# Optimization experiments

Hardware: AMD Instinct MI355X
Metric: run time of the kernel (lower is better)

## Reference

```python
import jax, jax.numpy as jnp
import numpy as np

HEADS = 16
LN_EPS = 1e-5

def _ln(v, w, b):
    # LayerNorm over last dim (head dim s)
    mu = jnp.mean(v, axis=-1, keepdims=True)
    var = jnp.mean(jnp.square(v - mu), axis=-1, keepdims=True)
    return (v - mu) * jax.lax.rsqrt(var + LN_EPS) * w + b

def setup_inputs() -> dict:
    key = jax.random.key(0)
    ks = jax.random.split(key, 5)
    b, t, e = 2, 2048, 1024
    x = jax.random.normal(ks[0], (b, t, e), dtype=jnp.float32)
    scale = 0.02
    Wk = jax.random.normal(ks[1], (e, e), dtype=jnp.float32) * scale
    Wq = jax.random.normal(ks[2], (e, e), dtype=jnp.float32) * scale
    Wv = jax.random.normal(ks[3], (e, e), dtype=jnp.float32) * scale
    Wu = jax.random.normal(ks[4], (e, e), dtype=jnp.float32) * scale
    s = e // HEADS
    return {
        "x": x, "Wk": Wk, "Wq": Wq, "Wv": Wv, "Wu": Wu,
        "kln_w": jnp.ones((s,), jnp.float32), "kln_b": jnp.zeros((s,), jnp.float32),
        "qln_w": jnp.ones((s,), jnp.float32), "qln_b": jnp.zeros((s,), jnp.float32),
    }

def reference(x, Wk, Wq, Wv, Wu, kln_w, kln_b, qln_w, qln_b):
    b, t, e = x.shape
    h = HEADS
    s = e // h
    # nn.Linear: y = x @ W^T
    k = (x @ Wk.T).reshape(b, t, h, s)
    q = (x @ Wq.T).reshape(b, t, h, s)
    v = (x @ Wv.T).reshape(b, t, h, s)
    k = _ln(k, kln_w, kln_b)
    q = _ln(q, qln_w, qln_b)
    scalefactor = 1.0 / np.sqrt(s).astype(np.float32)
    # [b, h, t_q, t_k]
    dot = jnp.einsum('bqhs,bkhs->bhqk', q, k) * scalefactor
    causal = jnp.triu(jnp.ones((t, t), dtype=bool), k=1)  # mask strictly-upper (diag kept)
    dot = jnp.where(causal, -jnp.inf, dot)
    attn = jax.nn.softmax(dot, axis=-1)
    out = jnp.einsum('bhqk,bkhs->bqhs', attn, v).reshape(b, t, e)
    return out @ Wu.T
```

## Files before the change

kernel.cpp:

```cpp
#include <hip/hip_runtime.h>
#include <math.h>

#define T_SEQ 2048
#define E_DIM 1024
#define NH    16
#define HS    64
#define NB    2
#define M_ROWS 4096

typedef __attribute__((ext_vector_type(8))) short bf16x8;
typedef __attribute__((ext_vector_type(4))) float f32x4;

#define AS1 __attribute__((address_space(1)))
#define AS3 __attribute__((address_space(3)))

#define LOG2E 1.4426950408889634f

__device__ __forceinline__ ushort f2bf(float f) {
    union { float f; unsigned u; } c; c.f = f;
    unsigned r = c.u + 0x7fffu + ((c.u >> 16) & 1u);
    return (ushort)(r >> 16);
}
__device__ __forceinline__ ushort f2bf_trunc(float f) {
    union { float f; unsigned u; } c; c.f = f;
    return (ushort)(c.u >> 16);
}

__device__ __forceinline__ void load_lds16(const ushort* g, ushort* l) {
    __builtin_amdgcn_global_load_lds((const AS1 unsigned int*)g,
                                     (AS3 unsigned int*)l, 16, 0, 0);
}

__global__ __launch_bounds__(256) void cvt_all(
    const float* __restrict__ x,  const float* __restrict__ Wk,
    const float* __restrict__ Wq, const float* __restrict__ Wv,
    const float* __restrict__ Wu,
    ushort* __restrict__ xb,  ushort* __restrict__ Wkb,
    ushort* __restrict__ Wqb, ushort* __restrict__ Wvb,
    ushort* __restrict__ Wub)
{
    int i4 = blockIdx.x * 256 + threadIdx.x;
    int region = i4 >> 18;
    const float* src; ushort* dst; int off;
    if      (region < 4)  { src = x;  dst = xb;  off = i4; }
    else if (region == 4) { src = Wk; dst = Wkb; off = i4 - (4 << 18); }
    else if (region == 5) { src = Wq; dst = Wqb; off = i4 - (5 << 18); }
    else if (region == 6) { src = Wv; dst = Wvb; off = i4 - (6 << 18); }
    else                  { src = Wu; dst = Wub; off = i4 - (7 << 18); }
    float4 v = *(const float4*)(src + (size_t)off * 4);
    ushort4 o; o.x = f2bf(v.x); o.y = f2bf(v.y); o.z = f2bf(v.z); o.w = f2bf(v.w);
    *(ushort4*)(dst + (size_t)off * 4) = o;
}

__device__ __forceinline__ void gemm_core64(
    const ushort* __restrict__ A, const ushort* __restrict__ W,
    int m0, int n0, ushort* As, ushort* Bs, f32x4 acc[2][4])
{
    const int tid  = threadIdx.x;
    const int lane = tid & 63, w = tid >> 6;
    const int quad = lane >> 4, l16 = lane & 15;

    const int rl   = lane >> 2;
    const int gsw  = (lane & 3) ^ ((lane >> 3) & 3);
    const int fsw  = (l16 >> 1) & 3;

    const f32x4 zero = {0.f, 0.f, 0.f, 0.f};
#pragma unroll
    for (int mt = 0; mt < 2; ++mt)
#pragma unroll
        for (int nt = 0; nt < 4; ++nt) acc[mt][nt] = zero;

    for (int k0 = 0; k0 < E_DIM; k0 += 32) {
#pragma unroll
        for (int i = 0; i < 2; ++i) {
            int c = w + i * 4;
            int row = c * 16 + rl;
            load_lds16(A + (size_t)(m0 + row) * E_DIM + k0 + gsw * 8, As + c * 512);
        }
        {
            int row = w * 16 + rl;
            load_lds16(W + (size_t)(n0 + row) * E_DIM + k0 + gsw * 8, Bs + w * 512);
        }
        __syncthreads();
        bf16x8 af[2], bfr[4];
#pragma unroll
        for (int mt = 0; mt < 2; ++mt)
            af[mt] = *(const bf16x8*)(As + (w * 32 + mt * 16 + l16) * 32
                                      + ((quad ^ fsw) * 8));
#pragma unroll
        for (int nt = 0; nt < 4; ++nt)
            bfr[nt] = *(const bf16x8*)(Bs + (nt * 16 + l16) * 32
                                       + ((quad ^ fsw) * 8));
#pragma unroll
        for (int mt = 0; mt < 2; ++mt)
#pragma unroll
            for (int nt = 0; nt < 4; ++nt)
                acc[mt][nt] = __builtin_amdgcn_mfma_f32_16x16x32_bf16(
                    af[mt], bfr[nt], acc[mt][nt], 0, 0, 0);
        __syncthreads();
    }
}

__global__ __launch_bounds__(256) void gemm_qkv(
    const ushort* __restrict__ A,
    const ushort* __restrict__ W0, const ushort* __restrict__ W1,
    const ushort* __restrict__ W2,
    ushort* __restrict__ Kb, ushort* __restrict__ Qb, ushort* __restrict__ Vt,
    const float* __restrict__ kw, const float* __restrict__ kbias,
    const float* __restrict__ qw, const float* __restrict__ qbias)
{
    __shared__ ushort As[128 * 32];
    __shared__ ushort Bs[64 * 32];
    const int n0g = blockIdx.x * 64;
    const int z   = n0g >> 10;
    const int n0  = n0g & 1023;
    const int m0  = blockIdx.y * 128;
    const ushort* W = (z == 0) ? W0 : (z == 1) ? W1 : W2;

    f32x4 acc[2][4];
    gemm_core64(A, W, m0, n0, As, Bs, acc);

    const int lane = threadIdx.x & 63, w = threadIdx.x >> 6;
    const int quad = lane >> 4, l16 = lane & 15;
    const int row0 = m0 + w * 32;

    if (z < 2) {
        ushort* C = z ? Qb : Kb;
        const float* lw = z ? qw : kw;
        const float* lb = z ? qbias : kbias;
        const float scale = z ? (0.125f * LOG2E) : 1.0f;
        float wv[4], bv_[4];
#pragma unroll
        for (int nt = 0; nt < 4; ++nt) {
            wv[nt]  = lw[nt * 16 + l16];
            bv_[nt] = lb[nt * 16 + l16];
        }
#pragma unroll
        for (int mt = 0; mt < 2; ++mt)
#pragma unroll
            for (int r = 0; r < 4; ++r) {
                float v[4], d[4];
#pragma unroll
                for (int nt = 0; nt < 4; ++nt) v[nt] = acc[mt][nt][r];
                float s = v[0] + v[1] + v[2] + v[3];
                s += __shfl_xor(s, 1); s += __shfl_xor(s, 2);
                s += __shfl_xor(s, 4); s += __shfl_xor(s, 8);
                float mu = s * (1.0f / 64.0f);
                float q2 = 0.f;
#pragma unroll
                for (int nt = 0; nt < 4; ++nt) { d[nt] = v[nt] - mu; q2 += d[nt] * d[nt]; }
                q2 += __shfl_xor(q2, 1); q2 += __shfl_xor(q2, 2);
                q2 += __shfl_xor(q2, 4); q2 += __shfl_xor(q2, 8);
                float rin = rsqrtf(q2 * (1.0f / 64.0f) + 1e-5f);
                int row = row0 + mt * 16 + quad * 4 + r;
#pragma unroll
                for (int nt = 0; nt < 4; ++nt)
                    C[(size_t)row * E_DIM + n0 + nt * 16 + l16] =
                        f2bf((d[nt] * rin * wv[nt] + bv_[nt]) * scale);
            }
    } else {
        const int bidx = m0 >> 11;
        const int hh   = n0 >> 6;
        const int t0   = (m0 & 2047) + w * 32;
#pragma unroll
        for (int mt = 0; mt < 2; ++mt)
#pragma unroll
            for (int nt = 0; nt < 4; ++nt) {
                ushort4 pk = make_ushort4(f2bf(acc[mt][nt][0]), f2bf(acc[mt][nt][1]),
                                          f2bf(acc[mt][nt][2]), f2bf(acc[mt][nt][3]));
                size_t off = ((size_t)(bidx * NH + hh) * 64 + nt * 16 + l16) * T_SEQ
                             + t0 + mt * 16 + quad * 4;
                *(ushort4*)(Vt + off) = pk;
            }
    }
}

__global__ __launch_bounds__(256) void gemm_o(
    const ushort* __restrict__ A, const ushort* __restrict__ W,
    float* __restrict__ C)
{
    __shared__ ushort As[128 * 32];
    __shared__ ushort Bs[64 * 32];
    const int m0 = blockIdx.y * 128, n0 = blockIdx.x * 64;
    f32x4 acc[2][4];
    gemm_core64(A, W, m0, n0, As, Bs, acc);

    const int lane = threadIdx.x & 63, w = threadIdx.x >> 6;
    const int quad = lane >> 4, l16 = lane & 15;
    const int row0 = m0 + w * 32;
#pragma unroll
    for (int mt = 0; mt < 2; ++mt)
#pragma unroll
        for (int nt = 0; nt < 4; ++nt)
#pragma unroll
            for (int r = 0; r < 4; ++r)
                C[(size_t)(row0 + mt * 16 + quad * 4 + r) * E_DIM
                  + n0 + nt * 16 + l16] = acc[mt][nt][r];
}

__global__ __launch_bounds__(256) void flash_attn4(
    const ushort* __restrict__ Qg, const ushort* __restrict__ Kg,
    const ushort* __restrict__ Vt, ushort* __restrict__ O)
{
    __shared__ ushort Ks[2][64 * 64];
    __shared__ ushort Vs[2][64 * 64];
    __shared__ ushort Ps[4][32 * 64];

    const int tid  = threadIdx.x;
    const int lane = tid & 63, w = tid >> 6;
    const int quad = lane >> 4, l16 = lane & 15;

    const int L = blockIdx.x;
    const int c = L & 255, s = L >> 8;
    const int q0 = c >> 5;
    const int bh = c & 31;
    const int qt = s ? (15 - q0) : q0;
    const int b = bh >> 4, h = bh & 15;

    const ushort* Qbase = Qg + ((size_t)b * T_SEQ) * E_DIM + h * HS;
    const ushort* Kbase = Kg + ((size_t)b * T_SEQ) * E_DIM + h * HS;
    const ushort* Vbase = Vt + ((size_t)bh * HS) * T_SEQ;

    const int rloc = lane >> 3;
    const int gswc = (lane & 7) ^ rloc;
    const int sw   = l16 & 7;

    const int base_w = qt * 128 + w * 32;

    bf16x8 aq[2][2];
#pragma unroll
    for (int u = 0; u < 2; ++u)
#pragma unroll
        for (int ks = 0; ks < 2; ++ks)
            aq[u][ks] = *(const bf16x8*)(Qbase
                + (size_t)(base_w + u * 16 + l16) * E_DIM + ks * 32 + quad * 8);

    const f32x4 zero = {0.f, 0.f, 0.f, 0.f};
    f32x4 o_acc[2][4];
#pragma unroll
    for (int u = 0; u < 2; ++u)
#pragma unroll
        for (int dt = 0; dt < 4; ++dt) o_acc[u][dt] = zero;
    float l_acc[2][4] = {{0.f,0.f,0.f,0.f},{0.f,0.f,0.f,0.f}};

#pragma unroll
    for (int i = 0; i < 2; ++i) {
        int cc = w * 2 + i, row = cc * 8 + rloc;
        load_lds16(Kbase + (size_t)row * E_DIM + gswc * 8, Ks[0] + cc * 512);
        load_lds16(Vbase + (size_t)row * T_SEQ + gswc * 8, Vs[0] + cc * 512);
    }

    const float M8 = 8.0f * LOG2E;
    const int ntiles = 2 * qt + 2;

    for (int jt = 0; jt < ntiles; ++jt) {
        const int buf = jt & 1;
        __syncthreads();
        if (jt + 1 < ntiles) {
#pragma unroll
            for (int i = 0; i < 2; ++i) {
                int cc = w * 2 + i, row = cc * 8 + rloc;
                load_lds16(Kbase + (size_t)(jt + 1) * 64 * E_DIM
                           + (size_t)row * E_DIM + gswc * 8, Ks[buf ^ 1] + cc * 512);
                load_lds16(Vbase + (size_t)row * T_SEQ + (jt + 1) * 64 + gswc * 8,
                           Vs[buf ^ 1] + cc * 512);
            }
        }

        if (jt * 64 > base_w + 31) continue;

        f32x4 sa[2][4];
#pragma unroll
        for (int u = 0; u < 2; ++u)
#pragma unroll
            for (int nt = 0; nt < 4; ++nt) sa[u][nt] = zero;
#pragma unroll
        for (int ks = 0; ks < 2; ++ks) {
            int cp = ((ks * 4 + quad) ^ sw) * 8;
            bf16x8 bk[4];
#pragma unroll
            for (int nt = 0; nt < 4; ++nt)
                bk[nt] = *(const bf16x8*)(Ks[buf] + (nt * 16 + l16) * 64 + cp);
#pragma unroll
            for (int u = 0; u < 2; ++u)
#pragma unroll
                for (int nt = 0; nt < 4; ++nt)
                    sa[u][nt] = __builtin_amdgcn_mfma_f32_16x16x32_bf16(
                        aq[u][ks], bk[nt], sa[u][nt], 0, 0, 0);
        }

        if (jt * 64 + 63 > base_w) {
#pragma unroll
            for (int u = 0; u < 2; ++u)
#pragma unroll
                for (int nt = 0; nt < 4; ++nt)
#pragma unroll
                    for (int r = 0; r < 4; ++r)
                        if (jt * 64 + nt * 16 + l16 >
                            base_w + u * 16 + quad * 4 + r) sa[u][nt][r] = -1e30f;
        }

#pragma unroll
        for (int u = 0; u < 2; ++u)
#pragma unroll
            for (int nt = 0; nt < 4; ++nt)
#pragma unroll
                for (int r = 0; r < 4; ++r) {
                    float p = __builtin_amdgcn_exp2f(sa[u][nt][r] - M8);
                    sa[u][nt][r] = p;
                    l_acc[u][r] += p;
                }

#pragma unroll
        for (int u = 0; u < 2; ++u)
#pragma unroll
            for (int nt = 0; nt < 4; ++nt)
#pragma unroll
                for (int r = 0; r < 4; ++r) {
                    int row = u * 16 + quad * 4 + r;
                    int cp2 = (nt * 2 + (l16 >> 3)) ^ (row & 7);
                    Ps[w][row * 64 + cp2 * 8 + (l16 & 7)] = f2bf_trunc(sa[u][nt][r]);
                }

#pragma unroll
        for (int ks = 0; ks < 2; ++ks) {
            int cp = ((ks * 4 + quad) ^ sw) * 8;
            bf16x8 bv[4];
#pragma unroll
            for (int dt = 0; dt < 4; ++dt)
                bv[dt] = *(const bf16x8*)(Vs[buf] + (dt * 16 + l16) * 64 + cp);
#pragma unroll
            for (int u = 0; u < 2; ++u) {
                bf16x8 ap = *(const bf16x8*)(Ps[w] + (u * 16 + l16) * 64 + cp);
#pragma unroll
                for (int dt = 0; dt < 4; ++dt)
                    o_acc[u][dt] = __builtin_amdgcn_mfma_f32_16x16x32_bf16(
                        ap, bv[dt], o_acc[u][dt], 0, 0, 0);
            }
        }
    }

#pragma unroll
    for (int u = 0; u < 2; ++u)
#pragma unroll
        for (int r = 0; r < 4; ++r) {
            float Lr = l_acc[u][r];
            Lr += __shfl_xor(Lr, 1); Lr += __shfl_xor(Lr, 2);
            Lr += __shfl_xor(Lr, 4); Lr += __shfl_xor(Lr, 8);
            float inv = 1.0f / Lr;
            int trow = base_w + u * 16 + quad * 4 + r;
#pragma unroll
            for (int dt = 0; dt < 4; ++dt)
                O[((size_t)b * T_SEQ + trow) * E_DIM + h * HS + dt * 16 + l16] =
                    f2bf(o_acc[u][dt][r] * inv);
        }
}

extern "C" void kernel_launch(void* const* d_in, const int* in_sizes, int n_in,
                              void* d_out, int out_size, void* d_ws, size_t ws_size,
                              hipStream_t stream) {
    const float* x     = (const float*)d_in[0];
    const float* Wk    = (const float*)d_in[1];
    const float* Wq    = (const float*)d_in[2];
    const float* Wv    = (const float*)d_in[3];
    const float* Wu    = (const float*)d_in[4];
    const float* kln_w = (const float*)d_in[5];
    const float* kln_b = (const float*)d_in[6];
    const float* qln_w = (const float*)d_in[7];
    const float* qln_b = (const float*)d_in[8];
    float* out = (float*)d_out;

    const size_t NE = (size_t)M_ROWS * E_DIM;
    const size_t NW = (size_t)E_DIM * E_DIM;
    ushort* xb  = (ushort*)d_ws;
    ushort* Wkb = xb  + NE;
    ushort* Wqb = Wkb + NW;
    ushort* Wvb = Wqb + NW;
    ushort* Wub = Wvb + NW;
    ushort* Kb  = Wub + NW;
    ushort* Qb  = Kb  + NE;
    ushort* Vt  = Qb  + NE;
    ushort* Ob  = Vt  + NE;

    cvt_all<<<8192, 256, 0, stream>>>(x, Wk, Wq, Wv, Wu, xb, Wkb, Wqb, Wvb, Wub);

    gemm_qkv<<<dim3(3 * E_DIM / 64, M_ROWS / 128), 256, 0, stream>>>(
        xb, Wkb, Wqb, Wvb, Kb, Qb, Vt, kln_w, kln_b, qln_w, qln_b);

    flash_attn4<<<512, 256, 0, stream>>>(Qb, Kb, Vt, Ob);

    gemm_o<<<dim3(E_DIM / 64, M_ROWS / 128), 256, 0, stream>>>(Ob, Wub, out);
}
```

Measured before the change: 204.9 us.

## Enlarge QKV GEMM tile to 128x128 with 2x2 warp layout, retile output GEMM

The QKV projection GEMM now uses 128x128 block tiles with a 2x2 wave arrangement, so each wave computes a 64x64 sub-tile. This raises arithmetic intensity per LDS load and halves the block count. The output projection keeps its 128x64 tile but switches to a 2x2 wave layout, where each wave computes 64x32, which improves fragment reuse. The trade-off is more accumulator registers per thread, which may lower occupancy, and fewer blocks for the QKV GEMM (768 vs 1536), which may hurt load balance.

```diff
diff --git a/kernel.cpp b/kernel.cpp
--- a/kernel.cpp
+++ b/kernel.cpp
@@ -52,13 +52,14 @@
     *(ushort4*)(dst + (size_t)off * 4) = o;
 }
 
-__device__ __forceinline__ void gemm_core64(
+__device__ __forceinline__ void gemm_core(
     const ushort* __restrict__ A, const ushort* __restrict__ W,
-    int m0, int n0, ushort* As, ushort* Bs, f32x4 acc[2][4])
+    int m0, int n0, ushort* As, ushort* Bs, f32x4 acc[4][4])
 {
     const int tid  = threadIdx.x;
     const int lane = tid & 63, w = tid >> 6;
     const int quad = lane >> 4, l16 = lane & 15;
+    const int wm = w & 1, wn = w >> 1;
 
     const int rl   = lane >> 2;
     const int gsw  = (lane & 3) ^ ((lane >> 3) & 3);
@@ -66,33 +67,30 @@
 
     const f32x4 zero = {0.f, 0.f, 0.f, 0.f};
 #pragma unroll
-    for (int mt = 0; mt < 2; ++mt)
+    for (int mt = 0; mt < 4; ++mt)
 #pragma unroll
         for (int nt = 0; nt < 4; ++nt) acc[mt][nt] = zero;
 
     for (int k0 = 0; k0 < E_DIM; k0 += 32) {
 #pragma unroll
         for (int i = 0; i < 2; ++i) {
-            int c = w + i * 4;
+            int c = i * 4 + w;
             int row = c * 16 + rl;
             load_lds16(A + (size_t)(m0 + row) * E_DIM + k0 + gsw * 8, As + c * 512);
-        }
-        {
-            int row = w * 16 + rl;
-            load_lds16(W + (size_t)(n0 + row) * E_DIM + k0 + gsw * 8, Bs + w * 512);
+            load_lds16(W + (size_t)(n0 + row) * E_DIM + k0 + gsw * 8, Bs + c * 512);
         }
         __syncthreads();
-        bf16x8 af[2], bfr[4];
-#pragma unroll
-        for (int mt = 0; mt < 2; ++mt)
-            af[mt] = *(const bf16x8*)(As + (w * 32 + mt * 16 + l16) * 32
+        bf16x8 af[4], bfr[4];
+#pragma unroll
+        for (int mt = 0; mt < 4; ++mt)
+            af[mt] = *(const bf16x8*)(As + (wm * 64 + mt * 16 + l16) * 32
                                       + ((quad ^ fsw) * 8));
 #pragma unroll
         for (int nt = 0; nt < 4; ++nt)
-            bfr[nt] = *(const bf16x8*)(Bs + (nt * 16 + l16) * 32
+            bfr[nt] = *(const bf16x8*)(Bs + (wn * 64 + nt * 16 + l16) * 32
                                        + ((quad ^ fsw) * 8));
 #pragma unroll
-        for (int mt = 0; mt < 2; ++mt)
+        for (int mt = 0; mt < 4; ++mt)
 #pragma unroll
             for (int nt = 0; nt < 4; ++nt)
                 acc[mt][nt] = __builtin_amdgcn_mfma_f32_16x16x32_bf16(
@@ -110,19 +108,18 @@
     const float* __restrict__ qw, const float* __restrict__ qbias)
 {
     __shared__ ushort As[128 * 32];
-    __shared__ ushort Bs[64 * 32];
-    const int n0g = blockIdx.x * 64;
-    const int z   = n0g >> 10;
-    const int n0  = n0g & 1023;
-    const int m0  = blockIdx.y * 128;
+    __shared__ ushort Bs[128 * 32];
+    const int z = blockIdx.z;
     const ushort* W = (z == 0) ? W0 : (z == 1) ? W1 : W2;
-
-    f32x4 acc[2][4];
-    gemm_core64(A, W, m0, n0, As, Bs, acc);
+    const int m0 = blockIdx.y * 128, n0 = blockIdx.x * 128;
+    f32x4 acc[4][4];
+    gemm_core(A, W, m0, n0, As, Bs, acc);
 
     const int lane = threadIdx.x & 63, w = threadIdx.x >> 6;
     const int quad = lane >> 4, l16 = lane & 15;
-    const int row0 = m0 + w * 32;
+    const int wm = w & 1, wn = w >> 1;
+    const int row0 = m0 + wm * 64;
+    const int col0 = n0 + wn * 64;
 
     if (z < 2) {
         ushort* C = z ? Qb : Kb;
@@ -136,7 +133,7 @@
             bv_[nt] = lb[nt * 16 + l16];
         }
 #pragma unroll
-        for (int mt = 0; mt < 2; ++mt)
+        for (int mt = 0; mt < 4; ++mt)
 #pragma unroll
             for (int r = 0; r < 4; ++r) {
                 float v[4], d[4];
@@ -155,15 +152,15 @@
                 int row = row0 + mt * 16 + quad * 4 + r;
 #pragma unroll
                 for (int nt = 0; nt < 4; ++nt)
-                    C[(size_t)row * E_DIM + n0 + nt * 16 + l16] =
+                    C[(size_t)row * E_DIM + col0 + nt * 16 + l16] =
                         f2bf((d[nt] * rin * wv[nt] + bv_[nt]) * scale);
             }
     } else {
         const int bidx = m0 >> 11;
-        const int hh   = n0 >> 6;
-        const int t0   = (m0 & 2047) + w * 32;
-#pragma unroll
-        for (int mt = 0; mt < 2; ++mt)
+        const int hh   = col0 >> 6;
+        const int t0   = (m0 & 2047) + wm * 64;
+#pragma unroll
+        for (int mt = 0; mt < 4; ++mt)
 #pragma unroll
             for (int nt = 0; nt < 4; ++nt) {
                 ushort4 pk = make_ushort4(f2bf(acc[mt][nt][0]), f2bf(acc[mt][nt][1]),
@@ -181,21 +178,63 @@
 {
     __shared__ ushort As[128 * 32];
     __shared__ ushort Bs[64 * 32];
+    const int tid  = threadIdx.x;
+    const int lane = tid & 63, w = tid >> 6;
+    const int quad = lane >> 4, l16 = lane & 15;
+    const int wm = w & 1, wn = w >> 1;
     const int m0 = blockIdx.y * 128, n0 = blockIdx.x * 64;
-    f32x4 acc[2][4];
-    gemm_core64(A, W, m0, n0, As, Bs, acc);
-
-    const int lane = threadIdx.x & 63, w = threadIdx.x >> 6;
-    const int quad = lane >> 4, l16 = lane & 15;
-    const int row0 = m0 + w * 32;
-#pragma unroll
-    for (int mt = 0; mt < 2; ++mt)
-#pragma unroll
-        for (int nt = 0; nt < 4; ++nt)
+
+    const int rl  = lane >> 2;
+    const int gsw = (lane & 3) ^ ((lane >> 3) & 3);
+    const int fsw = (l16 >> 1) & 3;
+
+    const f32x4 zero = {0.f, 0.f, 0.f, 0.f};
+    f32x4 acc[4][2];
+#pragma unroll
+    for (int mt = 0; mt < 4; ++mt)
+#pragma unroll
+        for (int nt = 0; nt < 2; ++nt) acc[mt][nt] = zero;
+
+    for (int k0 = 0; k0 < E_DIM; k0 += 32) {
+#pragma unroll
+        for (int i = 0; i < 2; ++i) {
+            int c = i * 4 + w;
+            int row = c * 16 + rl;
+            load_lds16(A + (size_t)(m0 + row) * E_DIM + k0 + gsw * 8, As + c * 512);
+        }
+        {
+            int row = w * 16 + rl;
+            load_lds16(W + (size_t)(n0 + row) * E_DIM + k0 + gsw * 8, Bs + w * 512);
+        }
+        __syncthreads();
+        bf16x8 af[4], bfr[2];
+#pragma unroll
+        for (int mt = 0; mt < 4; ++mt)
+            af[mt] = *(const bf16x8*)(As + (wm * 64 + mt * 16 + l16) * 32
+                                      + ((quad ^ fsw) * 8));
+#pragma unroll
+        for (int nt = 0; nt < 2; ++nt)
+            bfr[nt] = *(const bf16x8*)(Bs + (wn * 32 + nt * 16 + l16) * 32
+                                       + ((quad ^ fsw) * 8));
+#pragma unroll
+        for (int mt = 0; mt < 4; ++mt)
+#pragma unroll
+            for (int nt = 0; nt < 2; ++nt)
+                acc[mt][nt] = __builtin_amdgcn_mfma_f32_16x16x32_bf16(
+                    af[mt], bfr[nt], acc[mt][nt], 0, 0, 0);
+        __syncthreads();
+    }
+
+    const int row0 = m0 + wm * 64;
+    const int col0 = n0 + wn * 32;
+#pragma unroll
+    for (int mt = 0; mt < 4; ++mt)
+#pragma unroll
+        for (int nt = 0; nt < 2; ++nt)
 #pragma unroll
             for (int r = 0; r < 4; ++r)
                 C[(size_t)(row0 + mt * 16 + quad * 4 + r) * E_DIM
-                  + n0 + nt * 16 + l16] = acc[mt][nt][r];
+                  + col0 + nt * 16 + l16] = acc[mt][nt][r];
 }
 
 __global__ __launch_bounds__(256) void flash_attn4(
@@ -384,7 +423,7 @@
 
     cvt_all<<<8192, 256, 0, stream>>>(x, Wk, Wq, Wv, Wu, xb, Wkb, Wqb, Wvb, Wub);
 
-    gemm_qkv<<<dim3(3 * E_DIM / 64, M_ROWS / 128), 256, 0, stream>>>(
+    gemm_qkv<<<dim3(E_DIM / 128, M_ROWS / 128, 3), 256, 0, stream>>>(
         xb, Wkb, Wqb, Wvb, Kb, Qb, Vt, kln_w, kln_b, qln_w, qln_b);
 
     flash_attn4<<<512, 256, 0, stream>>>(Qb, Kb, Vt, Ob);
```

After: 190.8 us. 6.9% less time.
